# Optimization experiments

Measured on AMD Instinct MI355X. Metric: run time of the kernel, lower is better.

The kernel has to match this reference:

```python
import jax, jax.numpy as jnp
import numpy as np

E, D_IN, D_HID, D_OUT, N = 8, 1024, 2048, 1024, 8192


def setup_inputs() -> dict:
    key = jax.random.key(0)
    ks = jax.random.split(key, 9)
    s_in = 1.0 / np.sqrt(D_IN)
    s_hid = 1.0 / np.sqrt(D_HID)
    return {
        "x": jax.random.normal(ks[0], (N, D_IN), dtype=jnp.float32),
        "gW": jax.random.normal(ks[1], (D_IN, E), dtype=jnp.float32) * s_in,
        "gb": jnp.zeros((E,), dtype=jnp.float32),
        "W0": jax.random.normal(ks[2], (E, D_IN, D_HID), dtype=jnp.float32) * s_in,
        "b0": jax.random.normal(ks[3], (E, D_HID), dtype=jnp.float32) * 0.01,
        "W1": jax.random.normal(ks[4], (E, D_HID, D_HID), dtype=jnp.float32) * s_hid,
        "b1": jax.random.normal(ks[5], (E, D_HID), dtype=jnp.float32) * 0.01,
        "Wf": jax.random.normal(ks[6], (E, D_HID, D_OUT), dtype=jnp.float32) * s_hid,
        "bf": jax.random.normal(ks[7], (E, D_OUT), dtype=jnp.float32) * 0.01,
    }


def reference(x, gW, gb, W0, b0, W1, b1, Wf, bf):
    # gate: softmax over experts  [N, E]
    gate = jax.nn.softmax(x @ gW + gb, axis=-1)
    # all experts densely, batched over expert axis E
    h = jax.nn.relu(jnp.einsum("nd,edh->enh", x, W0) + b0[:, None, :])   # [E,N,H]
    h = jax.nn.relu(jnp.einsum("enh,ehk->enk", h, W1) + b1[:, None, :])  # [E,N,H]
    o = jnp.einsum("enh,eho->eno", h, Wf) + bf[:, None, :]               # [E,N,O]
    # gate-weighted sum over experts -> [N, O]
    return jnp.einsum("ne,eno->no", gate, o)
```

## Files before the change

### kernel.cpp

```cpp
#include <hip/hip_runtime.h>
#include <hip/hip_bf16.h>


typedef short s16x8 __attribute__((ext_vector_type(8)));
typedef float f32x4 __attribute__((ext_vector_type(4)));

#define E_ 8
#define DIN_ 1024
#define DH_ 2048
#define DOUT_ 1024
#define NTOK_ 8192

__device__ __forceinline__ unsigned short f2bf(float x) {
    union { float f; unsigned u; } c; c.f = x;
    unsigned r = c.u + 0x7fffu + ((c.u >> 16) & 1u);
    return (unsigned short)(r >> 16);
}
__device__ __forceinline__ float bf2f(unsigned short s) {
    union { unsigned u; float f; } c; c.u = ((unsigned)s) << 16;
    return c.f;
}
__device__ __forceinline__ void gload_lds16(const void* g, void* l) {
    __builtin_amdgcn_global_load_lds((const __attribute__((address_space(1))) void*)g,
                                     (__attribute__((address_space(3))) void*)l, 16, 0, 0);
}

__global__ __launch_bounds__(256) void cvt_f32_bf16(const float* __restrict__ in,
                                                    unsigned short* __restrict__ out,
                                                    long n8) {
    long i = (long)blockIdx.x * 256 + threadIdx.x;
    if (i >= n8) return;
    const float4* p = (const float4*)(in + i * 8);
    float4 a = p[0], b = p[1];
    s16x8 v;
    v[0] = (short)f2bf(a.x); v[1] = (short)f2bf(a.y);
    v[2] = (short)f2bf(a.z); v[3] = (short)f2bf(a.w);
    v[4] = (short)f2bf(b.x); v[5] = (short)f2bf(b.y);
    v[6] = (short)f2bf(b.z); v[7] = (short)f2bf(b.w);
    *(s16x8*)(out + i * 8) = v;
}

__global__ __launch_bounds__(256) void tcvt_kernel(const float* __restrict__ in,
                                                   unsigned short* __restrict__ out,
                                                   int K, int Nn) {
    __shared__ unsigned short t[64][72];
    const int e = blockIdx.z;
    const float* ie = in + (long)e * K * Nn;
    unsigned short* oe = out + (long)e * K * Nn;
    const int k0 = blockIdx.y * 64, n0 = blockIdx.x * 64;
    const int tid = threadIdx.x;
    const int c4 = (tid & 15) * 4;
#pragma unroll
    for (int i = 0; i < 4; ++i) {
        const int k = (tid >> 4) + 16 * i;
        float4 v = *(const float4*)(ie + (long)(k0 + k) * Nn + n0 + c4);
        t[c4 + 0][k] = f2bf(v.x);
        t[c4 + 1][k] = f2bf(v.y);
        t[c4 + 2][k] = f2bf(v.z);
        t[c4 + 3][k] = f2bf(v.w);
    }
    __syncthreads();
#pragma unroll
    for (int i = 0; i < 2; ++i) {
        const int idx = tid + 256 * i;
        const int rn = idx >> 3, ck = idx & 7;
        s16x8 v = *(const s16x8*)&t[rn][ck * 8];
        *(s16x8*)(oe + (long)(n0 + rn) * K + k0 + ck * 8) = v;
    }
}

__global__ __launch_bounds__(256) void gate_kernel(const float* __restrict__ x,
                                                   const float* __restrict__ gW,
                                                   const float* __restrict__ gb,
                                                   float* __restrict__ gate) {
    __shared__ float gws[8 * 1024];
    const int tid = threadIdx.x;
    for (int idx = tid; idx < 8 * 1024; idx += 256)
        gws[(idx & 7) * 1024 + (idx >> 3)] = gW[idx];
    __syncthreads();
    const int w = tid >> 6, l = tid & 63;
    const int n = blockIdx.x * 4 + w;
    const float* xr = x + (long)n * 1024;
    float acc[8] = {};
    for (int k = l; k < 1024; k += 64) {
        const float xv = xr[k];
#pragma unroll
        for (int e = 0; e < 8; ++e) acc[e] += xv * gws[e * 1024 + k];
    }
#pragma unroll
    for (int e = 0; e < 8; ++e)
        for (int off = 32; off > 0; off >>= 1) acc[e] += __shfl_xor(acc[e], off);
    if (l == 0) {
        float m = -1e30f;
#pragma unroll
        for (int e = 0; e < 8; ++e) { acc[e] += gb[e]; m = fmaxf(m, acc[e]); }
        float s = 0.f;
#pragma unroll
        for (int e = 0; e < 8; ++e) { acc[e] = __expf(acc[e] - m); s += acc[e]; }
        const float inv = 1.0f / s;
#pragma unroll
        for (int e = 0; e < 8; ++e) gate[n * 8 + e] = acc[e] * inv;
    }
}


#define BARR() asm volatile("s_barrier" ::: "memory")
#define LGKM0() do { asm volatile("s_waitcnt lgkmcnt(0)" ::: "memory"); \
                     __builtin_amdgcn_sched_barrier(0); } while (0)
#define VMW(n) do { asm volatile("s_waitcnt vmcnt(" #n ")" ::: "memory"); \
                    __builtin_amdgcn_sched_barrier(0); } while (0)

__global__ __launch_bounds__(512, 2) void moe_gemm256(const unsigned short* __restrict__ A,
                                                      const unsigned short* __restrict__ Bt,
                                                      const float* __restrict__ bias,
                                                      unsigned short* __restrict__ out,
                                                      int M, int Nn, int K,
                                                      long sAe, long sBe, long sOe, int relu) {
    extern __shared__ char smem[];
    const int tid = threadIdx.x;
    const int l = tid & 63, wid = tid >> 6;
    const int wr = wid >> 2, wc = wid & 3;
    const int e = blockIdx.z;
    const int gx = gridDim.x;
    int lin = blockIdx.x + gx * blockIdx.y;
    {
        const int nwg = gx * gridDim.y;
        const int q = nwg >> 3, r = nwg & 7;
        const int xcd = lin & 7, idx = lin >> 3;
        lin = (xcd < r ? xcd * (q + 1) : r * (q + 1) + (xcd - r) * q) + idx;
    }
    const int n0 = (lin % gx) * 256;
    const int m0 = (lin / gx) * 256;

    const unsigned short* Ae = A + (long)e * sAe;
    const unsigned short* Be = Bt + (long)e * sBe;

    const int srow = wid * 8 + (l >> 3);
    const int sc8 = ((l & 7) ^ (l >> 3)) * 8;
    const unsigned short* pA = Ae + (long)(m0 + srow) * K + sc8;
    const unsigned short* pB = Be + (long)(n0 + srow) * K + sc8;
    const long kst64 = 64L * K;
    char* ldsW = smem + wid * 1024;

#define STAGE_A(buf, half, kt) do { \
        const unsigned short* s_ = pA + (long)(half) * 128 * K + (long)(kt) * 64; \
        char* d_ = ldsW + (buf) * 65536 + (half) * 16384; \
        gload_lds16(s_, d_); gload_lds16(s_ + kst64, d_ + 8192); } while (0)
#define STAGE_B(buf, half, kt) do { \
        const unsigned short* s_ = pB + (long)(half) * 128 * K + (long)(kt) * 64; \
        char* d_ = ldsW + (buf) * 65536 + 32768 + (half) * 16384; \
        gload_lds16(s_, d_); gload_lds16(s_ + kst64, d_ + 8192); } while (0)

    const int arow = l & 15;
    const int aswz = ((l >> 4) ^ (l & 7)) << 4;
    const int aoffb = wr * 16384 + arow * 128;
    const int boffb = 32768 + wc * 8192 + arow * 128;

    f32x4 acc[8][4] = {};
    s16x8 af[4][2], bf0[2][2], bf1[2][2];

#define LDA(buf, mhalf) do { \
        const char* p_ = smem + (buf) * 65536 + aoffb + (mhalf) * 8192; \
        _Pragma("unroll") for (int mi_ = 0; mi_ < 4; ++mi_) \
        _Pragma("unroll") for (int kk_ = 0; kk_ < 2; ++kk_) \
            af[mi_][kk_] = *(const s16x8*)(p_ + mi_ * 2048 + (aswz ^ (kk_ << 6))); } while (0)
#define LDB(buf, nhalf, dst) do { \
        const char* p_ = smem + (buf) * 65536 + boffb + (nhalf) * 4096; \
        _Pragma("unroll") for (int ni_ = 0; ni_ < 2; ++ni_) \
        _Pragma("unroll") for (int kk_ = 0; kk_ < 2; ++kk_) \
            dst[ni_][kk_] = *(const s16x8*)(p_ + ni_ * 2048 + (aswz ^ (kk_ << 6))); } while (0)
#define MFMA8(mb, nb, bfr) do { __builtin_amdgcn_s_setprio(1); \
        _Pragma("unroll") for (int mi_ = 0; mi_ < 4; ++mi_) \
        _Pragma("unroll") for (int ni_ = 0; ni_ < 2; ++ni_) \
        _Pragma("unroll") for (int kk_ = 0; kk_ < 2; ++kk_) \
            acc[(mb) + mi_][(nb) + ni_] = __builtin_amdgcn_mfma_f32_16x16x32_bf16( \
                af[mi_][kk_], bfr[ni_][kk_], acc[(mb) + mi_][(nb) + ni_], 0, 0, 0); \
        __builtin_amdgcn_s_setprio(0); } while (0)

    const int nit = K >> 7;

    STAGE_A(0, 0, 0); STAGE_A(0, 1, 0); STAGE_B(0, 0, 0); STAGE_B(0, 1, 0);
    STAGE_B(1, 0, 1); STAGE_A(1, 0, 1);
    VMW(4); BARR();

    for (int it = 0; it < nit; ++it) {
        const int ktY = 2 * it + 1;
        const int ktX2 = (it + 1 < nit) ? 2 * it + 2 : 0;
        const int ktY2 = (it + 1 < nit) ? 2 * it + 3 : 1;
        LDA(0, 0); LDB(0, 0, bf0);
        STAGE_A(1, 1, ktY);
        BARR(); LGKM0(); MFMA8(0, 0, bf0); BARR();
        LDB(0, 1, bf1);
        STAGE_B(1, 1, ktY);
        BARR(); LGKM0(); MFMA8(0, 2, bf1); BARR();
        LDA(0, 1);
        STAGE_B(0, 0, ktX2);
        BARR(); LGKM0(); MFMA8(4, 2, bf1); BARR();
        STAGE_B(0, 1, ktX2);
        BARR(); MFMA8(4, 0, bf0); VMW(4); BARR();
        LDA(1, 0); LDB(1, 0, bf0);
        STAGE_A(0, 0, ktX2);
        BARR(); LGKM0(); MFMA8(0, 0, bf0); BARR();
        LDB(1, 1, bf1);
        STAGE_A(0, 1, ktX2);
        BARR(); LGKM0(); MFMA8(0, 2, bf1); BARR();
        LDA(1, 1);
        STAGE_B(1, 0, ktY2);
        BARR(); LGKM0(); MFMA8(4, 2, bf1); BARR();
        STAGE_A(1, 0, ktY2);
        BARR(); MFMA8(4, 0, bf0); VMW(4); BARR();
    }
    VMW(0); BARR();

    unsigned short* oe = out + (long)e * sOe;
    const float* be = bias + (long)e * Nn;
    float bv[4];
#pragma unroll
    for (int ni = 0; ni < 4; ++ni) bv[ni] = be[n0 + 64 * wc + 16 * ni + arow];
    unsigned short (*h)[272] = (unsigned short (*)[272])smem;
#pragma unroll
    for (int p = 0; p < 2; ++p) {
        if (p) BARR();
        if (wr == p) {
#pragma unroll
            for (int mi = 0; mi < 8; ++mi)
#pragma unroll
                for (int ni = 0; ni < 4; ++ni) {
                    const int col = 64 * wc + 16 * ni + arow;
                    const int rl = 16 * mi + (l >> 4) * 4;
#pragma unroll
                    for (int j = 0; j < 4; ++j) {
                        float xv = acc[mi][ni][j] + bv[ni];
                        if (relu) xv = fmaxf(xv, 0.0f);
                        h[rl + j][col] = f2bf(xv);
                    }
                }
        }
        BARR();
#pragma unroll
        for (int i = 0; i < 8; ++i) {
            const int lin2 = i * 512 + tid;
            const int row = lin2 >> 5, ch = (lin2 & 31) * 8;
            s16x8 v = *(const s16x8*)&h[row][ch];
            *(s16x8*)(oe + (long)(m0 + 128 * p + row) * Nn + n0 + ch) = v;
        }
    }
#undef STAGE_A
#undef STAGE_B
#undef LDA
#undef LDB
#undef MFMA8
}

template <int FUSE>
__global__ __launch_bounds__(256) void moe_gemm(const unsigned short* __restrict__ A,
                                                const unsigned short* __restrict__ Bt,
                                                const float* __restrict__ bias,
                                                void* __restrict__ outp,
                                                const float* __restrict__ gate8,
                                                int M, int Nn, int K,
                                                long strideAe, long strideBe, long strideOe,
                                                int relu, int first) {
    __shared__ __align__(16) char smem[34816];
    const int tid = threadIdx.x;
    const int w = tid >> 6, l = tid & 63;
    const int e = blockIdx.z;
    const int m0 = blockIdx.y * 128;
    const int n0 = blockIdx.x * 128;

    const unsigned short* Ae = A + (long)e * strideAe;
    const unsigned short* Be = Bt + (long)e * strideBe;

    const int srow = tid >> 2;
    const int scol = (tid & 3) * 8;
    const unsigned short* gA = Ae + (long)(m0 + srow) * K + scol;
    const unsigned short* gB = Be + (long)(n0 + srow) * K + scol;
    const long rstep = (long)64 * K;

    char* ldsAw = smem + w * 1024;
    char* ldsBw = smem + 8192 + w * 1024;

    const int wr = w >> 1, wc = w & 1;
    const int lr = l & 15;
    const int aoff = (64 * wr + lr) * 64 + (l >> 4) * 16;
    const int boff = 8192 + (64 * wc + lr) * 64 + (l >> 4) * 16;

    f32x4 acc[4][4] = {};
    const int nt = K >> 5;

    gload_lds16(gA, ldsAw);
    gload_lds16(gA + rstep, ldsAw + 4096);
    gload_lds16(gB, ldsBw);
    gload_lds16(gB + rstep, ldsBw + 4096);
    __syncthreads();

    int cur = 0;
    for (int t = 0; t < nt; ++t) {
        if (t + 1 < nt) {
            const int nb = (cur ^ 1) * 16384;
            const unsigned short* a = gA + (t + 1) * 32;
            const unsigned short* b = gB + (t + 1) * 32;
            gload_lds16(a, ldsAw + nb);
            gload_lds16(a + rstep, ldsAw + nb + 4096);
            gload_lds16(b, ldsBw + nb);
            gload_lds16(b + rstep, ldsBw + nb + 4096);
        }
        const char* buf = smem + cur * 16384;
        s16x8 af[4], bfr[4];
#pragma unroll
        for (int m = 0; m < 4; ++m) af[m] = *(const s16x8*)(buf + aoff + m * 1024);
#pragma unroll
        for (int n = 0; n < 4; ++n) bfr[n] = *(const s16x8*)(buf + boff + n * 1024);
#pragma unroll
        for (int m = 0; m < 4; ++m)
#pragma unroll
            for (int n = 0; n < 4; ++n)
                acc[m][n] = __builtin_amdgcn_mfma_f32_16x16x32_bf16(af[m], bfr[n], acc[m][n], 0, 0, 0);
        __syncthreads();
        cur ^= 1;
    }

    const float* be = bias + (long)e * Nn;

    if constexpr (!FUSE) {
        unsigned short (*h)[136] = (unsigned short (*)[136])smem;
#pragma unroll
        for (int n = 0; n < 4; ++n) {
            const int lc = 64 * wc + 16 * n + lr;
            const float bb = be[n0 + lc];
#pragma unroll
            for (int m = 0; m < 4; ++m) {
                const int rbase = 64 * wr + 16 * m + (l >> 4) * 4;
                f32x4 v = acc[m][n];
#pragma unroll
                for (int j = 0; j < 4; ++j) {
                    float xv = v[j] + bb;
                    if (relu) xv = fmaxf(xv, 0.0f);
                    h[rbase + j][lc] = f2bf(xv);
                }
            }
        }
        __syncthreads();
        unsigned short* oe = (unsigned short*)outp + (long)e * strideOe;
#pragma unroll
        for (int it = 0; it < 8; ++it) {
            const int row = (tid >> 4) + 16 * it;
            const int ch = tid & 15;
            s16x8 v = *(const s16x8*)&h[row][ch * 8];
            *(s16x8*)(oe + (long)(m0 + row) * Nn + n0 + ch * 8) = v;
        }
    } else {
        float* outf = (float*)outp;
        float (*h2)[132] = (float (*)[132])smem;
#pragma unroll
        for (int p2 = 0; p2 < 2; ++p2) {
            if (p2) __syncthreads();
            if (wr == p2) {
#pragma unroll
                for (int n = 0; n < 4; ++n) {
                    const int lc = 64 * wc + 16 * n + lr;
                    const float bb = be[n0 + lc];
#pragma unroll
                    for (int m = 0; m < 4; ++m) {
                        const int rloc = 16 * m + (l >> 4) * 4;
                        f32x4 v = acc[m][n];
#pragma unroll
                        for (int j = 0; j < 4; ++j) h2[rloc + j][lc] = v[j] + bb;
                    }
                }
            }
            __syncthreads();
#pragma unroll
            for (int it = 0; it < 8; ++it) {
                const int lin = it * 256 + tid;
                const int row = lin >> 5;
                const int c4 = (lin & 31) * 4;
                const long grow = (long)m0 + p2 * 64 + row;
                const float g = gate8[grow * 8];
                float* op = outf + grow * Nn + n0 + c4;
                float4 hv = *(const float4*)&h2[row][c4];
                float4 r;
                if (first) {
                    r = make_float4(g * hv.x, g * hv.y, g * hv.z, g * hv.w);
                } else {
                    float4 o0 = *(const float4*)op;
                    r = make_float4(o0.x + g * hv.x, o0.y + g * hv.y,
                                    o0.z + g * hv.z, o0.w + g * hv.w);
                }
                *(float4*)op = r;
            }
        }
    }
}

__global__ __launch_bounds__(256) void combine_kernel(const unsigned short* __restrict__ o,
                                                      const float* __restrict__ gate,
                                                      float* __restrict__ out, int Nc) {
    const long t = (long)blockIdx.x * 256 + threadIdx.x;
    const int n = (int)(t >> 7);
    const int ch = (int)(t & 127) * 8;
    float g[8];
#pragma unroll
    for (int e = 0; e < 8; ++e) g[e] = gate[n * 8 + e];
    float a[8] = {};
#pragma unroll
    for (int e = 0; e < 8; ++e) {
        s16x8 v = *(const s16x8*)(o + (long)e * Nc * DOUT_ + (long)n * DOUT_ + ch);
        const float ge = g[e];
#pragma unroll
        for (int j = 0; j < 8; ++j) a[j] = fmaf(ge, bf2f((unsigned short)v[j]), a[j]);
    }
    float* op = out + (long)n * DOUT_ + ch;
    *(float4*)(op) = make_float4(a[0], a[1], a[2], a[3]);
    *(float4*)(op + 4) = make_float4(a[4], a[5], a[6], a[7]);
}

extern "C" void kernel_launch(void* const* d_in, const int* in_sizes, int n_in,
                              void* d_out, int out_size, void* d_ws, size_t ws_size,
                              hipStream_t stream) {
    const float* x   = (const float*)d_in[0];
    const float* gW  = (const float*)d_in[1];
    const float* gb  = (const float*)d_in[2];
    const float* W0  = (const float*)d_in[3];
    const float* b0  = (const float*)d_in[4];
    const float* W1  = (const float*)d_in[5];
    const float* b1  = (const float*)d_in[6];
    const float* Wf  = (const float*)d_in[7];
    const float* bfb = (const float*)d_in[8];
    float* out = (float*)d_out;
    char* ws = (char*)d_ws;

    unsigned short* xb = (unsigned short*)ws;
    float* gate = (float*)(ws + (size_t)NTOK_ * DIN_ * 2);
    const size_t base = (size_t)NTOK_ * DIN_ * 2 + (size_t)NTOK_ * E_ * 4;

    const size_t wfull = (size_t)E_ * 2 * ((size_t)DIN_ * DH_ + (size_t)DH_ * DH_ + (size_t)DH_ * DOUT_);
    const size_t wexp = wfull / E_;

    int Nc = 0, batched = 0;
    if (ws_size > base + wfull) {
        const size_t rem = ws_size - base - wfull;
        for (int nc = 8192; nc >= 256; nc >>= 1)
            if ((size_t)nc * 65536 <= rem) { Nc = nc; batched = 1; break; }
    }
    if (!batched) {
        const size_t rem = (ws_size > base + wexp) ? ws_size - base - wexp : 0;
        for (int nc = 8192; nc >= 128; nc >>= 1)
            if ((size_t)nc * 8192 <= rem) { Nc = nc; break; }
        if (!Nc) Nc = 128;
    }
    const int nch = NTOK_ / Nc;

    cvt_f32_bf16<<<NTOK_ * DIN_ / 8 / 256, 256, 0, stream>>>(x, xb, (long)NTOK_ * DIN_ / 8);
    gate_kernel<<<NTOK_ / 4, 256, 0, stream>>>(x, gW, gb, gate);

    if (batched) {
        hipFuncSetAttribute(reinterpret_cast<const void*>(&moe_gemm256),
                            hipFuncAttributeMaxDynamicSharedMemorySize, 131072);
        unsigned short* W0b = (unsigned short*)(ws + base);
        unsigned short* W1b = W0b + (size_t)E_ * DIN_ * DH_;
        unsigned short* Wfb = W1b + (size_t)E_ * DH_ * DH_;
        unsigned short* h0  = Wfb + (size_t)E_ * DH_ * DOUT_;
        unsigned short* h1  = h0 + (size_t)E_ * Nc * DH_;
        tcvt_kernel<<<dim3(DH_ / 64, DIN_ / 64, E_), 256, 0, stream>>>(W0, W0b, DIN_, DH_);
        tcvt_kernel<<<dim3(DH_ / 64, DH_ / 64, E_), 256, 0, stream>>>(W1, W1b, DH_, DH_);
        tcvt_kernel<<<dim3(DOUT_ / 64, DH_ / 64, E_), 256, 0, stream>>>(Wf, Wfb, DH_, DOUT_);
        for (int c = 0; c < nch; ++c) {
            const long r0 = (long)c * Nc;
            moe_gemm256<<<dim3(DH_ / 256, Nc / 256, E_), 512, 131072, stream>>>(
                xb + r0 * DIN_, W0b, b0, h0, Nc, DH_, DIN_,
                0L, (long)DIN_ * DH_, (long)Nc * DH_, 1);
            moe_gemm256<<<dim3(DH_ / 256, Nc / 256, E_), 512, 131072, stream>>>(
                h0, W1b, b1, h1, Nc, DH_, DH_,
                (long)Nc * DH_, (long)DH_ * DH_, (long)Nc * DH_, 1);
            unsigned short* o = h0;
            moe_gemm256<<<dim3(DOUT_ / 256, Nc / 256, E_), 512, 131072, stream>>>(
                h1, Wfb, bfb, o, Nc, DOUT_, DH_,
                (long)Nc * DH_, (long)DH_ * DOUT_, (long)Nc * DOUT_, 0);
            combine_kernel<<<Nc / 2, 256, 0, stream>>>(o, gate + r0 * E_, out + r0 * DOUT_, Nc);
        }
    } else {
        unsigned short* W0s = (unsigned short*)(ws + base);
        unsigned short* W1s = W0s + (size_t)DIN_ * DH_;
        unsigned short* Wfs = W1s + (size_t)DH_ * DH_;
        unsigned short* h0s = Wfs + (size_t)DH_ * DOUT_;
        unsigned short* h1s = h0s + (size_t)Nc * DH_;
        for (int e = 0; e < E_; ++e) {
            tcvt_kernel<<<dim3(DH_ / 64, DIN_ / 64, 1), 256, 0, stream>>>(
                W0 + (size_t)e * DIN_ * DH_, W0s, DIN_, DH_);
            tcvt_kernel<<<dim3(DH_ / 64, DH_ / 64, 1), 256, 0, stream>>>(
                W1 + (size_t)e * DH_ * DH_, W1s, DH_, DH_);
            tcvt_kernel<<<dim3(DOUT_ / 64, DH_ / 64, 1), 256, 0, stream>>>(
                Wf + (size_t)e * DH_ * DOUT_, Wfs, DH_, DOUT_);
            for (int c = 0; c < nch; ++c) {
                const long r0 = (long)c * Nc;
                moe_gemm<0><<<dim3(DH_ / 128, Nc / 128, 1), 256, 0, stream>>>(
                    xb + r0 * DIN_, W0s, b0 + e * DH_, h0s, nullptr, Nc, DH_, DIN_,
                    0L, 0L, 0L, 1, 0);
                moe_gemm<0><<<dim3(DH_ / 128, Nc / 128, 1), 256, 0, stream>>>(
                    h0s, W1s, b1 + e * DH_, h1s, nullptr, Nc, DH_, DH_,
                    0L, 0L, 0L, 1, 0);
                moe_gemm<1><<<dim3(DOUT_ / 128, Nc / 128, 1), 256, 0, stream>>>(
                    h1s, Wfs, bfb + e * DOUT_, out + r0 * DOUT_, gate + r0 * E_ + e,
                    Nc, DOUT_, DH_, 0L, 0L, 0L, 0, (e == 0) ? 1 : 0);
            }
        }
    }
}
```

Measured before the change: 1.144 ms.

## Software-pipeline GEMM main loop: overlap LDS reads and staging with MFMA, fewer barriers

Restructures the K-loop of the expert GEMM so that LDS fragment loads and global-to-LDS staging are issued after, and overlap with, the MFMA blocks instead of being bracketed by barriers on both sides. The first fragment loads are hoisted before the loop and the next iteration's are issued at the end of each iteration. A sched_barrier after each MFMA group pins the compiler's ordering. This roughly halves the workgroup barriers per iteration, at the risk of LDS read/write hazards if buffer reuse ordering is wrong and of higher register pressure.

```diff
diff --git a/kernel.cpp b/kernel.cpp
--- a/kernel.cpp
+++ b/kernel.cpp
@@ -175,42 +175,50 @@
         _Pragma("unroll") for (int kk_ = 0; kk_ < 2; ++kk_) \
             acc[(mb) + mi_][(nb) + ni_] = __builtin_amdgcn_mfma_f32_16x16x32_bf16( \
                 af[mi_][kk_], bfr[ni_][kk_], acc[(mb) + mi_][(nb) + ni_], 0, 0, 0); \
-        __builtin_amdgcn_s_setprio(0); } while (0)
+        __builtin_amdgcn_s_setprio(0); __builtin_amdgcn_sched_barrier(0); } while (0)
 
     const int nit = K >> 7;
 
     STAGE_A(0, 0, 0); STAGE_A(0, 1, 0); STAGE_B(0, 0, 0); STAGE_B(0, 1, 0);
     STAGE_B(1, 0, 1); STAGE_A(1, 0, 1);
-    VMW(4); BARR();
+    VMW(4);
+    BARR();
+    LDA(0, 0); LDB(0, 0, bf0);
 
     for (int it = 0; it < nit; ++it) {
         const int ktY = 2 * it + 1;
         const int ktX2 = (it + 1 < nit) ? 2 * it + 2 : 0;
         const int ktY2 = (it + 1 < nit) ? 2 * it + 3 : 1;
+        LGKM0(); MFMA8(0, 0, bf0);
+        STAGE_A(1, 1, ktY);
+        LDB(0, 1, bf1);
+        BARR(); LGKM0(); MFMA8(0, 2, bf1);
+        STAGE_B(1, 1, ktY);
+        LDA(0, 1);
+        BARR(); LGKM0(); MFMA8(4, 2, bf1);
+        STAGE_B(0, 0, ktX2);
+        BARR(); MFMA8(4, 0, bf0);
+        STAGE_B(0, 1, ktX2);
+        VMW(4);
+        BARR();
+        LDA(1, 0); LDB(1, 0, bf0);
+        LGKM0(); MFMA8(0, 0, bf0);
+        STAGE_A(0, 0, ktX2);
+        LDB(1, 1, bf1);
+        BARR(); LGKM0(); MFMA8(0, 2, bf1);
+        STAGE_A(0, 1, ktX2);
+        LDA(1, 1);
+        BARR(); LGKM0(); MFMA8(4, 2, bf1);
+        STAGE_B(1, 0, ktY2);
+        BARR(); MFMA8(4, 0, bf0);
+        STAGE_A(1, 0, ktY2);
+        VMW(4);
+        BARR();
         LDA(0, 0); LDB(0, 0, bf0);
-        STAGE_A(1, 1, ktY);
-        BARR(); LGKM0(); MFMA8(0, 0, bf0); BARR();
-        LDB(0, 1, bf1);
-        STAGE_B(1, 1, ktY);
-        BARR(); LGKM0(); MFMA8(0, 2, bf1); BARR();
-        LDA(0, 1);
-        STAGE_B(0, 0, ktX2);
-        BARR(); LGKM0(); MFMA8(4, 2, bf1); BARR();
-        STAGE_B(0, 1, ktX2);
-        BARR(); MFMA8(4, 0, bf0); VMW(4); BARR();
-        LDA(1, 0); LDB(1, 0, bf0);
-        STAGE_A(0, 0, ktX2);
-        BARR(); LGKM0(); MFMA8(0, 0, bf0); BARR();
-        LDB(1, 1, bf1);
-        STAGE_A(0, 1, ktX2);
-        BARR(); LGKM0(); MFMA8(0, 2, bf1); BARR();
-        LDA(1, 1);
-        STAGE_B(1, 0, ktY2);
-        BARR(); LGKM0(); MFMA8(4, 2, bf1); BARR();
-        STAGE_A(1, 0, ktY2);
-        BARR(); MFMA8(4, 0, bf0); VMW(4); BARR();
-    }
-    VMW(0); BARR();
+    }
+    LGKM0();
+    VMW(0);
+    BARR();
 
     unsigned short* oe = out + (long)e * sOe;
     const float* be = bias + (long)e * Nn;
```

After: 1.126 ms (median of 2 runs). About the same (-1.6%).
